# Kernel tuning notes

Hardware: AMD Instinct MI355X
Metric: run time of the kernel (lower is better)

The kernel has to match this reference:

```python
import jax, jax.numpy as jnp
import numpy as np

C = 256
NUM_HEADS = 4
REDUCTION = 4
RED = C // REDUCTION           # 64
HEAD_DIM = RED // NUM_HEADS    # 16
SCALE = HEAD_DIM ** -0.5
LN_EPS = 1e-5


def setup_inputs() -> dict:
    key = jax.random.key(0)
    ks = jax.random.split(key, 9)
    B, H, W = 2, 64, 64
    x = jax.random.normal(ks[0], (B, C, H, W), dtype=jnp.float32)
    # LayerNorm params
    norm_w = jnp.ones((C,), jnp.float32)
    norm_b = jnp.zeros((C,), jnp.float32)
    # Linear weights (torch layout: [out, in]), y = x @ W.T
    qkv_w = jax.random.normal(ks[1], (3 * RED, C), jnp.float32) * (C ** -0.5)
    out_w = jax.random.normal(ks[2], (C, RED), jnp.float32) * (RED ** -0.5)
    # 1x1 conv weights, stored as [out_c, in_c]
    conv1_w = jax.random.normal(ks[3], (C // 2, C), jnp.float32) * (C ** -0.5)
    conv1_b = jax.random.normal(ks[4], (C // 2,), jnp.float32) * 0.01
    conv2_w = jax.random.normal(ks[5], (1, C // 2), jnp.float32) * ((C // 2) ** -0.5)
    conv2_b = jax.random.normal(ks[6], (1,), jnp.float32) * 0.01
    gamma = jnp.ones((1,), jnp.float32) * 0.5  # nonzero so output depends on attention
    return {"x": x, "norm_w": norm_w, "norm_b": norm_b, "qkv_w": qkv_w,
            "out_w": out_w, "conv1_w": conv1_w, "conv1_b": conv1_b,
            "conv2_w": conv2_w, "conv2_b": conv2_b, "gamma": gamma}


def reference(x, norm_w, norm_b, qkv_w, out_w, conv1_w, conv1_b, conv2_w, conv2_b, gamma):
    B, C_, H, W = x.shape
    N = H * W
    # [B, N, C]
    xf = x.reshape(B, C_, N).transpose(0, 2, 1)
    # LayerNorm over channel dim
    mu = jnp.mean(xf, axis=-1, keepdims=True)
    var = jnp.mean(jnp.square(xf - mu), axis=-1, keepdims=True)
    xn = (xf - mu) * jax.lax.rsqrt(var + LN_EPS) * norm_w + norm_b
    # QKV projection -> [B, N, 3*RED]
    qkv = jnp.einsum('bnc,oc->bno', xn, qkv_w)
    q, k, v = jnp.split(qkv, 3, axis=-1)
    def heads(t):  # [B, N, RED] -> [B, h, N, d]
        return t.reshape(B, N, NUM_HEADS, HEAD_DIM).transpose(0, 2, 1, 3)
    q, k, v = heads(q), heads(k), heads(v)
    attn = jax.nn.softmax(jnp.einsum('bhnd,bhmd->bhnm', q, k) * SCALE, axis=-1)
    # dynamic weight branch: two 1x1 convs on raw x
    d1 = jax.nn.relu(jnp.einsum('oc,bchw->bohw', conv1_w, x) + conv1_b[None, :, None, None])
    dyn = (jnp.einsum('oc,bchw->bohw', conv2_w, d1) + conv2_b[None, :, None, None])  # [B,1,H,W]
    dyn = dyn.reshape(B, 1, N)  # broadcast over heads
    # per-query row scaling of attention
    attn = attn * dyn[:, :, :, None]
    out = jnp.einsum('bhnm,bhmd->bhnd', attn, v)            # [B,h,N,d]
    out = out.transpose(0, 2, 1, 3).reshape(B, N, RED)      # [B,N,RED]
    out = jnp.einsum('bnr,cr->bnc', out, out_w)             # [B,N,C]
    out = out.transpose(0, 2, 1).reshape(B, C_, H, W)
    return jax.nn.sigmoid(gamma[0] * out + x)
```

## Files before the change

### kernel.cpp

```cpp
#include <hip/hip_runtime.h>
#include <cstdint>
#include <cstddef>

#define LOG2E 1.44269504088896340736f

typedef float  f32x16 __attribute__((ext_vector_type(16)));
typedef __bf16 bf16x8 __attribute__((ext_vector_type(8)));

union BF8 { bf16x8 v; uint u[4]; ushort us[8]; };

__device__ __forceinline__ uint pack_bf(float a, float b) {
    uint ua = __float_as_uint(a) + 0x8000u;
    uint ub = __float_as_uint(b) + 0x8000u;
    return __builtin_amdgcn_perm(ub, ua, 0x07060302u);
}
__device__ __forceinline__ uint cvt_pk_bf(float a, float b) {
    uint r;
    asm("v_cvt_pk_bf16_f32 %0, %1, %2" : "=v"(r) : "v"(a), "v"(b));
    return r;
}
__device__ __forceinline__ float bf_lo(uint u) { return __uint_as_float(u << 16); }
__device__ __forceinline__ float bf_hi(uint u) { return __uint_as_float(u & 0xFFFF0000u); }

__global__ __launch_bounds__(256) void convert_w_kernel(
    const float* __restrict__ qkv_w, const float* __restrict__ c1w,
    const float* __restrict__ out_w,
    ushort* __restrict__ qkvw_b, ushort* __restrict__ c1w_b, ushort* __restrict__ ow_b)
{
    const int g = (blockIdx.x * 256 + threadIdx.x) * 4;
    const float* src; ushort* dst; int off; float sc = 1.f;
    if (g < 49152)      { src = qkv_w; dst = qkvw_b; off = g;
                          if (g < 16384) sc = 0.25f * LOG2E; }
    else if (g < 81920) { src = c1w;   dst = c1w_b;  off = g - 49152; }
    else                { src = out_w; dst = ow_b;   off = g - 81920; }
    float4 v = *(const float4*)(src + off);
    uint2 pk;
    pk.x = pack_bf(v.x * sc, v.y * sc);
    pk.y = pack_bf(v.z * sc, v.w * sc);
    *(uint2*)(dst + off) = pk;
}

__global__ __launch_bounds__(1024) void lnqkv_kernel(
    const float* __restrict__ x, const float* __restrict__ nw, const float* __restrict__ nb,
    const ushort* __restrict__ qkvw_b, const ushort* __restrict__ c1w_b,
    const float* __restrict__ c1b, const float* __restrict__ c2w,
    const float* __restrict__ c2b,
    ushort* __restrict__ Qb, ushort* __restrict__ Kb, ushort* __restrict__ Vsw,
    float* __restrict__ dynb)
{
    __shared__ union {
        struct {
            uint  XN[32 * 32 * 4];
            uint  XR[32 * 32 * 4];
            float red1[1024];
            float red2[1024];
        } p;
        float trans[10][33 * 32];
    } S;
    __shared__ float muS[32], rsS[32];
    __shared__ float dpart[4][32];

    const int t    = threadIdx.x;
    const int pg   = blockIdx.x;
    const int b    = pg >> 7;
    const int n0   = (pg & 127) * 32;

    {
        const int j  = t & 31;
        const int cg = t >> 5;
        const size_t xb = (size_t)b * 256 * 4096 + n0 + j;
        float v[8];
        #pragma unroll
        for (int i = 0; i < 8; ++i) v[i] = x[xb + (size_t)(cg * 8 + i) * 4096];
        float s1 = 0.f, s2 = 0.f;
        #pragma unroll
        for (int i = 0; i < 8; ++i) { s1 += v[i]; s2 += v[i] * v[i]; }
        uint4 pk;
        pk.x = pack_bf(v[0], v[1]); pk.y = pack_bf(v[2], v[3]);
        pk.z = pack_bf(v[4], v[5]); pk.w = pack_bf(v[6], v[7]);
        *(uint4*)&S.p.XR[(cg * 32 + j) * 4] = pk;
        S.p.red1[t] = s1; S.p.red2[t] = s2;
        __syncthreads();
        if (t < 32) {
            float a = 0.f, q = 0.f;
            #pragma unroll 8
            for (int g2 = 0; g2 < 32; ++g2) { a += S.p.red1[g2 * 32 + t]; q += S.p.red2[g2 * 32 + t]; }
            float mu  = a * (1.f / 256.f);
            float var = q * (1.f / 256.f) - mu * mu;
            muS[t] = mu; rsS[t] = rsqrtf(fmaxf(var, 0.f) + 1e-5f);
        }
        __syncthreads();
        const float mu = muS[j], rs = rsS[j];
        const float4 w0 = *(const float4*)(nw + cg * 8);
        const float4 w1 = *(const float4*)(nw + cg * 8 + 4);
        const float4 b0 = *(const float4*)(nb + cg * 8);
        const float4 b1 = *(const float4*)(nb + cg * 8 + 4);
        float e0 = (v[0] - mu) * rs * w0.x + b0.x;
        float e1 = (v[1] - mu) * rs * w0.y + b0.y;
        float e2 = (v[2] - mu) * rs * w0.z + b0.z;
        float e3 = (v[3] - mu) * rs * w0.w + b0.w;
        float e4 = (v[4] - mu) * rs * w1.x + b1.x;
        float e5 = (v[5] - mu) * rs * w1.y + b1.y;
        float e6 = (v[6] - mu) * rs * w1.z + b1.z;
        float e7 = (v[7] - mu) * rs * w1.w + b1.w;
        uint4 o;
        o.x = pack_bf(e0, e1); o.y = pack_bf(e2, e3);
        o.z = pack_bf(e4, e5); o.w = pack_bf(e6, e7);
        *(uint4*)&S.p.XN[(cg * 32 + j) * 4] = o;
    }
    __syncthreads();

    const int w    = t >> 6;
    const int lane = t & 63;
    const int m    = lane & 31;
    const int h    = lane >> 5;
    const ushort* xnB = (const ushort*)S.p.XN;
    const ushort* xrB = (const ushort*)S.p.XR;

    f32x16 acc;
    #pragma unroll
    for (int i = 0; i < 16; ++i) acc[i] = 0.f;

    if (w < 6) {
        const int qkv = w >> 1;
        const int ti  = w & 1;
        const ushort* ap = qkvw_b + (size_t)(qkv * 64 + ti * 32 + m) * 256 + h * 8;
        #pragma unroll 4
        for (int ks = 0; ks < 16; ++ks) {
            bf16x8 bf = *(const bf16x8*)(xnB + ((ks * 2 + h) * 32 + m) * 8);
            bf16x8 af = *(const bf16x8*)(ap + ks * 16);
            acc = __builtin_amdgcn_mfma_f32_32x32x16_bf16(af, bf, acc, 0, 0, 0);
        }
    } else if (w < 10) {
        const int ti = w - 6;
        const ushort* ap = c1w_b + (size_t)(ti * 32 + m) * 256 + h * 8;
        #pragma unroll 4
        for (int ks = 0; ks < 16; ++ks) {
            bf16x8 bf = *(const bf16x8*)(xrB + ((ks * 2 + h) * 32 + m) * 8);
            bf16x8 af = *(const bf16x8*)(ap + ks * 16);
            acc = __builtin_amdgcn_mfma_f32_32x32x16_bf16(af, bf, acc, 0, 0, 0);
        }
    }
    __syncthreads();

    if (w < 10) {
        float* tr = S.trans[w];
        #pragma unroll
        for (int r = 0; r < 16; ++r)
            tr[((r & 3) + 8 * (r >> 2) + 4 * h) * 33 + m] = acc[r];

        if (w < 4) {
            const int qkv = w >> 1, ti = w & 1;
            ushort* dst = (qkv == 0) ? Qb : Kb;
            #pragma unroll
            for (int it = 0; it < 2; ++it) {
                int unit = it * 2 + h;
                int hl = unit >> 1, half = unit & 1;
                float v0 = tr[(hl * 16 + half * 8 + 0) * 33 + m];
                float v1 = tr[(hl * 16 + half * 8 + 1) * 33 + m];
                float v2 = tr[(hl * 16 + half * 8 + 2) * 33 + m];
                float v3 = tr[(hl * 16 + half * 8 + 3) * 33 + m];
                float v4 = tr[(hl * 16 + half * 8 + 4) * 33 + m];
                float v5 = tr[(hl * 16 + half * 8 + 5) * 33 + m];
                float v6 = tr[(hl * 16 + half * 8 + 6) * 33 + m];
                float v7 = tr[(hl * 16 + half * 8 + 7) * 33 + m];
                uint4 pk;
                pk.x = pack_bf(v0, v1); pk.y = pack_bf(v2, v3);
                pk.z = pack_bf(v4, v5); pk.w = pack_bf(v6, v7);
                int head = ti * 2 + hl;
                *(uint4*)(dst + ((size_t)(b * 4 + head) * 4096 + n0 + m) * 16 + half * 8) = pk;
            }
        } else if (w < 6) {
            const int ti = w & 1;
            int d = lane & 15, u = lane >> 4;
            #pragma unroll
            for (int it = 0; it < 4; ++it) {
                int unit = it * 4 + u;
                int hl = unit >> 3, sg = unit & 7;
                float v0 = tr[(hl * 16 + d) * 33 + sg * 4 + 0];
                float v1 = tr[(hl * 16 + d) * 33 + sg * 4 + 1];
                float v2 = tr[(hl * 16 + d) * 33 + sg * 4 + 2];
                float v3 = tr[(hl * 16 + d) * 33 + sg * 4 + 3];
                uint2 pk; pk.x = pack_bf(v0, v1); pk.y = pack_bf(v2, v3);
                int head = ti * 2 + hl;
                *(uint2*)(Vsw + (((size_t)(b * 4 + head) * 1024 + (pg & 127) * 8 + sg) * 16 + d) * 4) = pk;
            }
        } else {
            const int ti = w - 6;
            float partial = 0.f;
            #pragma unroll
            for (int i = 0; i < 16; ++i) {
                int og = ti * 32 + h * 16 + i;
                partial += fmaxf(tr[(h * 16 + i) * 33 + m] + c1b[og], 0.f) * c2w[og];
            }
            float tot = partial + __shfl_xor(partial, 32);
            if (lane < 32) dpart[ti][m] = tot;
        }
    }
    __syncthreads();
    if (t < 32)
        dynb[(size_t)b * 4096 + n0 + t] =
            c2b[0] + dpart[0][t] + dpart[1][t] + dpart[2][t] + dpart[3][t];
}

__global__ __launch_bounds__(1024, 4) void attn_final_kernel(
    const ushort* __restrict__ Qb, const ushort* __restrict__ Kb,
    const ushort* __restrict__ Vsw, const float* __restrict__ dynb,
    const ushort* __restrict__ ow_b, const float* __restrict__ x,
    const float* __restrict__ gamma, float* __restrict__ out)
{
    __shared__ float2 OM[4][4][8][32];
    __shared__ float  LM[4][4][32];

    const int t    = threadIdx.x;
    const int w    = t >> 6;
    const int lane = t & 63;
    const int c    = lane & 31;
    const int h    = lane >> 5;
    const int hd   = w & 3;
    const int kb   = w >> 2;
    const int pg   = blockIdx.x;
    const int b    = pg >> 7;
    const int n0   = (pg & 127) * 32;
    const int bh   = b * 4 + hd;

    const bf16x8 qf = *(const bf16x8*)(Qb + ((size_t)bh * 4096 + n0 + c) * 16 + h * 8);

    f32x16 oacc, zf;
    #pragma unroll
    for (int i = 0; i < 16; ++i) { oacc[i] = 0.f; zf[i] = 0.f; }

    const ushort* kp = Kb + ((size_t)bh * 4096 + kb * 1024 + c) * 16 + h * 8;
    const ushort* vb = Vsw + (size_t)bh * 65536 + ((size_t)kb * 256 + h) * 64 + c * 4;

    BF8 cones;
    {
        const uint f = (c == 16) ? 0x3F803F80u : 0u;
        cones.u[0] = f; cones.u[1] = f; cones.u[2] = f; cones.u[3] = f;
    }

    bf16x8 k0 = *(const bf16x8*)kp; kp += 512;
    bf16x8 k1 = *(const bf16x8*)kp; kp += 512;
    bf16x8 k2 = *(const bf16x8*)kp; kp += 512;
    bf16x8 k3 = *(const bf16x8*)kp; kp += 512;
    uint2 vA0 = *(const uint2*)(vb),       vB0 = *(const uint2*)(vb + 128);
    uint2 vC0 = *(const uint2*)(vb + 256), vD0 = *(const uint2*)(vb + 384);
    vb += 512;
    uint2 vA1 = *(const uint2*)(vb),       vB1 = *(const uint2*)(vb + 128);
    uint2 vC1 = *(const uint2*)(vb + 256), vD1 = *(const uint2*)(vb + 384);
    vb += 512;

#define STEP(K, VA, VB, VC, VD)                                                      \
    {                                                                                \
        __builtin_amdgcn_s_setprio(1);                                               \
        f32x16 s = __builtin_amdgcn_mfma_f32_32x32x16_bf16(K, qf, zf, 0, 0, 0);      \
        __builtin_amdgcn_s_setprio(0);                                               \
        K = *(const bf16x8*)kp; kp += 512;                                           \
        BF8 p1, p2;                                                                  \
        p1.u[0] = cvt_pk_bf(__builtin_amdgcn_exp2f(s[0]),  __builtin_amdgcn_exp2f(s[1]));  \
        p1.u[1] = cvt_pk_bf(__builtin_amdgcn_exp2f(s[2]),  __builtin_amdgcn_exp2f(s[3]));  \
        p1.u[2] = cvt_pk_bf(__builtin_amdgcn_exp2f(s[4]),  __builtin_amdgcn_exp2f(s[5]));  \
        p1.u[3] = cvt_pk_bf(__builtin_amdgcn_exp2f(s[6]),  __builtin_amdgcn_exp2f(s[7]));  \
        p2.u[0] = cvt_pk_bf(__builtin_amdgcn_exp2f(s[8]),  __builtin_amdgcn_exp2f(s[9]));  \
        p2.u[1] = cvt_pk_bf(__builtin_amdgcn_exp2f(s[10]), __builtin_amdgcn_exp2f(s[11])); \
        p2.u[2] = cvt_pk_bf(__builtin_amdgcn_exp2f(s[12]), __builtin_amdgcn_exp2f(s[13])); \
        p2.u[3] = cvt_pk_bf(__builtin_amdgcn_exp2f(s[14]), __builtin_amdgcn_exp2f(s[15])); \
        BF8 a1, a2;                                                                  \
        if (c < 16) {                                                                \
            a1.u[0] = VA.x; a1.u[1] = VA.y; a1.u[2] = VB.x; a1.u[3] = VB.y;          \
            a2.u[0] = VC.x; a2.u[1] = VC.y; a2.u[2] = VD.x; a2.u[3] = VD.y;          \
        } else { a1 = cones; a2 = cones; }                                           \
        VA = *(const uint2*)(vb);       VB = *(const uint2*)(vb + 128);              \
        VC = *(const uint2*)(vb + 256); VD = *(const uint2*)(vb + 384);              \
        vb += 512;                                                                   \
        __builtin_amdgcn_s_setprio(1);                                               \
        oacc = __builtin_amdgcn_mfma_f32_32x32x16_bf16(a1.v, p1.v, oacc, 0, 0, 0);   \
        oacc = __builtin_amdgcn_mfma_f32_32x32x16_bf16(a2.v, p2.v, oacc, 0, 0, 0);   \
        __builtin_amdgcn_s_setprio(0);                                               \
    }

    for (int it = 0; it < 8; ++it) {
        STEP(k0, vA0, vB0, vC0, vD0);
        STEP(k1, vA1, vB1, vC1, vD1);
        STEP(k2, vA0, vB0, vC0, vD0);
        STEP(k3, vA1, vB1, vC1, vD1);
    }
#undef STEP

    OM[kb][hd][2 * h + 0][c] = make_float2(oacc[0], oacc[1]);
    OM[kb][hd][2 * h + 1][c] = make_float2(oacc[2], oacc[3]);
    OM[kb][hd][4 + 2 * h][c] = make_float2(oacc[4], oacc[5]);
    OM[kb][hd][5 + 2 * h][c] = make_float2(oacc[6], oacc[7]);
    if (h == 0) LM[kb][hd][c] = oacc[8];
    __syncthreads();

    if (w < 8) {
        const int m = c;
        const float dyn_px = dynb[(size_t)b * 4096 + n0 + m];

        f32x16 acc;
        #pragma unroll
        for (int i = 0; i < 16; ++i) acc[i] = 0.f;

        #pragma unroll
        for (int ks = 0; ks < 4; ++ks) {
            float l = LM[0][ks][m] + LM[1][ks][m] + LM[2][ks][m] + LM[3][ks][m];
            float fac = dyn_px / l;
            BF8 bfr;
            #pragma unroll
            for (int i = 0; i < 4; ++i) {
                int sl = 4 * h + i;
                float2 s0 = OM[0][ks][sl][m];
                float2 s1 = OM[1][ks][sl][m];
                float2 s2 = OM[2][ks][sl][m];
                float2 s3 = OM[3][ks][sl][m];
                float e0 = (s0.x + s1.x + s2.x + s3.x) * fac;
                float e1 = (s0.y + s1.y + s2.y + s3.y) * fac;
                bfr.u[i] = pack_bf(e0, e1);
            }
            bf16x8 af = *(const bf16x8*)(ow_b + (size_t)(w * 32 + m) * 64 + ks * 16 + h * 8);
            acc = __builtin_amdgcn_mfma_f32_32x32x16_bf16(af, bfr.v, acc, 0, 0, 0);
        }

        const float g = gamma[0];
        #pragma unroll
        for (int r = 0; r < 16; ++r) {
            int o = (r & 3) + 8 * (r >> 2) + 4 * h;
            size_t idx = ((size_t)b * 256 + w * 32 + o) * 4096 + n0 + m;
            float z = g * acc[r] + x[idx];
            out[idx] = 1.f / (1.f + __builtin_amdgcn_exp2f(-z * LOG2E));
        }
    }
}

extern "C" void kernel_launch(void* const* d_in, const int* in_sizes, int n_in,
                              void* d_out, int out_size, void* d_ws, size_t ws_size,
                              hipStream_t stream)
{
    const float* x      = (const float*)d_in[0];
    const float* norm_w = (const float*)d_in[1];
    const float* norm_b = (const float*)d_in[2];
    const float* qkv_w  = (const float*)d_in[3];
    const float* out_w  = (const float*)d_in[4];
    const float* c1w    = (const float*)d_in[5];
    const float* c1b    = (const float*)d_in[6];
    const float* c2w    = (const float*)d_in[7];
    const float* c2b    = (const float*)d_in[8];
    const float* gamma  = (const float*)d_in[9];

    char* ws = (char*)d_ws;
    ushort* Qb     = (ushort*)ws;
    ushort* Kb     = Qb + 524288;
    ushort* Vsw    = Kb + 524288;
    ushort* qkvw_b = Vsw + 524288;
    ushort* c1w_b  = qkvw_b + 49152;
    ushort* ow_b   = c1w_b + 32768;
    float*  dynb   = (float*)(ws + 3342336);

    hipLaunchKernelGGL(convert_w_kernel, dim3(96), dim3(256), 0, stream,
                       qkv_w, c1w, out_w, qkvw_b, c1w_b, ow_b);
    hipLaunchKernelGGL(lnqkv_kernel, dim3(256), dim3(1024), 0, stream,
                       x, norm_w, norm_b, qkvw_b, c1w_b, c1b, c2w, c2b,
                       Qb, Kb, Vsw, dynb);
    hipLaunchKernelGGL(attn_final_kernel, dim3(256), dim3(1024), 0, stream,
                       Qb, Kb, Vsw, dynb, ow_b, x, gamma, (float*)d_out);
}
```

Baseline: 113.5 us.

## Fuse LN/QKV and attention kernels into one cooperative launch with grid sync

Merges the LayerNorm+QKV projection kernel and the attention+output kernel into a single cooperative kernel separated by a grid-wide barrier, with shared memory for both phases overlaid in a union. This removes one kernel launch and the inter-kernel gap. In exchange, all 256 blocks of 1024 threads must be co-resident, and a grid sync plus threadfence is added. The attention phase's occupancy hint of 4 blocks per CU now also constrains the first phase's register budget.

```diff
diff --git a/kernel.cpp b/kernel.cpp
--- a/kernel.cpp
+++ b/kernel.cpp
@@ -1,6 +1,9 @@
 #include <hip/hip_runtime.h>
+#include <hip/hip_cooperative_groups.h>
 #include <cstdint>
 #include <cstddef>
+
+namespace cg = cooperative_groups;
 
 #define LOG2E 1.44269504088896340736f
 
@@ -19,8 +22,6 @@
     asm("v_cvt_pk_bf16_f32 %0, %1, %2" : "=v"(r) : "v"(a), "v"(b));
     return r;
 }
-__device__ __forceinline__ float bf_lo(uint u) { return __uint_as_float(u << 16); }
-__device__ __forceinline__ float bf_hi(uint u) { return __uint_as_float(u & 0xFFFF0000u); }
 
 __global__ __launch_bounds__(256) void convert_w_kernel(
     const float* __restrict__ qkv_w, const float* __restrict__ c1w,
@@ -40,295 +41,294 @@
     *(uint2*)(dst + off) = pk;
 }
 
-__global__ __launch_bounds__(1024) void lnqkv_kernel(
+__global__ __launch_bounds__(1024, 4) void fused_kernel(
     const float* __restrict__ x, const float* __restrict__ nw, const float* __restrict__ nb,
     const ushort* __restrict__ qkvw_b, const ushort* __restrict__ c1w_b,
     const float* __restrict__ c1b, const float* __restrict__ c2w,
     const float* __restrict__ c2b,
     ushort* __restrict__ Qb, ushort* __restrict__ Kb, ushort* __restrict__ Vsw,
-    float* __restrict__ dynb)
+    float* __restrict__ dynb,
+    const ushort* __restrict__ ow_b, const float* __restrict__ gamma,
+    float* __restrict__ out)
 {
     __shared__ union {
         struct {
-            uint  XN[32 * 32 * 4];
-            uint  XR[32 * 32 * 4];
-            float red1[1024];
-            float red2[1024];
-        } p;
-        float trans[10][33 * 32];
-    } S;
-    __shared__ float muS[32], rsS[32];
-    __shared__ float dpart[4][32];
+            union {
+                struct {
+                    uint  XN[32 * 32 * 4];
+                    uint  XR[32 * 32 * 4];
+                    float red1[1024];
+                    float red2[1024];
+                } p;
+                float trans[10][33 * 32];
+            } S;
+            float muS[32], rsS[32];
+            float dpart[4][32];
+        } ln;
+        struct {
+            float2 OM[4][4][8][32];
+            float  LM[4][4][32];
+        } at;
+    } U;
 
     const int t    = threadIdx.x;
     const int pg   = blockIdx.x;
     const int b    = pg >> 7;
     const int n0   = (pg & 127) * 32;
-
-    {
-        const int j  = t & 31;
-        const int cg = t >> 5;
-        const size_t xb = (size_t)b * 256 * 4096 + n0 + j;
-        float v[8];
-        #pragma unroll
-        for (int i = 0; i < 8; ++i) v[i] = x[xb + (size_t)(cg * 8 + i) * 4096];
-        float s1 = 0.f, s2 = 0.f;
-        #pragma unroll
-        for (int i = 0; i < 8; ++i) { s1 += v[i]; s2 += v[i] * v[i]; }
-        uint4 pk;
-        pk.x = pack_bf(v[0], v[1]); pk.y = pack_bf(v[2], v[3]);
-        pk.z = pack_bf(v[4], v[5]); pk.w = pack_bf(v[6], v[7]);
-        *(uint4*)&S.p.XR[(cg * 32 + j) * 4] = pk;
-        S.p.red1[t] = s1; S.p.red2[t] = s2;
-        __syncthreads();
-        if (t < 32) {
-            float a = 0.f, q = 0.f;
-            #pragma unroll 8
-            for (int g2 = 0; g2 < 32; ++g2) { a += S.p.red1[g2 * 32 + t]; q += S.p.red2[g2 * 32 + t]; }
-            float mu  = a * (1.f / 256.f);
-            float var = q * (1.f / 256.f) - mu * mu;
-            muS[t] = mu; rsS[t] = rsqrtf(fmaxf(var, 0.f) + 1e-5f);
-        }
-        __syncthreads();
-        const float mu = muS[j], rs = rsS[j];
-        const float4 w0 = *(const float4*)(nw + cg * 8);
-        const float4 w1 = *(const float4*)(nw + cg * 8 + 4);
-        const float4 b0 = *(const float4*)(nb + cg * 8);
-        const float4 b1 = *(const float4*)(nb + cg * 8 + 4);
-        float e0 = (v[0] - mu) * rs * w0.x + b0.x;
-        float e1 = (v[1] - mu) * rs * w0.y + b0.y;
-        float e2 = (v[2] - mu) * rs * w0.z + b0.z;
-        float e3 = (v[3] - mu) * rs * w0.w + b0.w;
-        float e4 = (v[4] - mu) * rs * w1.x + b1.x;
-        float e5 = (v[5] - mu) * rs * w1.y + b1.y;
-        float e6 = (v[6] - mu) * rs * w1.z + b1.z;
-        float e7 = (v[7] - mu) * rs * w1.w + b1.w;
-        uint4 o;
-        o.x = pack_bf(e0, e1); o.y = pack_bf(e2, e3);
-        o.z = pack_bf(e4, e5); o.w = pack_bf(e6, e7);
-        *(uint4*)&S.p.XN[(cg * 32 + j) * 4] = o;
-    }
-    __syncthreads();
-
     const int w    = t >> 6;
     const int lane = t & 63;
     const int m    = lane & 31;
     const int h    = lane >> 5;
-    const ushort* xnB = (const ushort*)S.p.XN;
-    const ushort* xrB = (const ushort*)S.p.XR;
-
-    f32x16 acc;
-    #pragma unroll
-    for (int i = 0; i < 16; ++i) acc[i] = 0.f;
-
-    if (w < 6) {
-        const int qkv = w >> 1;
-        const int ti  = w & 1;
-        const ushort* ap = qkvw_b + (size_t)(qkv * 64 + ti * 32 + m) * 256 + h * 8;
-        #pragma unroll 4
-        for (int ks = 0; ks < 16; ++ks) {
-            bf16x8 bf = *(const bf16x8*)(xnB + ((ks * 2 + h) * 32 + m) * 8);
-            bf16x8 af = *(const bf16x8*)(ap + ks * 16);
-            acc = __builtin_amdgcn_mfma_f32_32x32x16_bf16(af, bf, acc, 0, 0, 0);
-        }
-    } else if (w < 10) {
-        const int ti = w - 6;
-        const ushort* ap = c1w_b + (size_t)(ti * 32 + m) * 256 + h * 8;
-        #pragma unroll 4
-        for (int ks = 0; ks < 16; ++ks) {
-            bf16x8 bf = *(const bf16x8*)(xrB + ((ks * 2 + h) * 32 + m) * 8);
-            bf16x8 af = *(const bf16x8*)(ap + ks * 16);
-            acc = __builtin_amdgcn_mfma_f32_32x32x16_bf16(af, bf, acc, 0, 0, 0);
-        }
-    }
-    __syncthreads();
-
-    if (w < 10) {
-        float* tr = S.trans[w];
-        #pragma unroll
-        for (int r = 0; r < 16; ++r)
-            tr[((r & 3) + 8 * (r >> 2) + 4 * h) * 33 + m] = acc[r];
-
-        if (w < 4) {
-            const int qkv = w >> 1, ti = w & 1;
-            ushort* dst = (qkv == 0) ? Qb : Kb;
-            #pragma unroll
-            for (int it = 0; it < 2; ++it) {
-                int unit = it * 2 + h;
-                int hl = unit >> 1, half = unit & 1;
-                float v0 = tr[(hl * 16 + half * 8 + 0) * 33 + m];
-                float v1 = tr[(hl * 16 + half * 8 + 1) * 33 + m];
-                float v2 = tr[(hl * 16 + half * 8 + 2) * 33 + m];
-                float v3 = tr[(hl * 16 + half * 8 + 3) * 33 + m];
-                float v4 = tr[(hl * 16 + half * 8 + 4) * 33 + m];
-                float v5 = tr[(hl * 16 + half * 8 + 5) * 33 + m];
-                float v6 = tr[(hl * 16 + half * 8 + 6) * 33 + m];
-                float v7 = tr[(hl * 16 + half * 8 + 7) * 33 + m];
-                uint4 pk;
-                pk.x = pack_bf(v0, v1); pk.y = pack_bf(v2, v3);
-                pk.z = pack_bf(v4, v5); pk.w = pack_bf(v6, v7);
-                int head = ti * 2 + hl;
-                *(uint4*)(dst + ((size_t)(b * 4 + head) * 4096 + n0 + m) * 16 + half * 8) = pk;
-            }
-        } else if (w < 6) {
-            const int ti = w & 1;
-            int d = lane & 15, u = lane >> 4;
-            #pragma unroll
-            for (int it = 0; it < 4; ++it) {
-                int unit = it * 4 + u;
-                int hl = unit >> 3, sg = unit & 7;
-                float v0 = tr[(hl * 16 + d) * 33 + sg * 4 + 0];
-                float v1 = tr[(hl * 16 + d) * 33 + sg * 4 + 1];
-                float v2 = tr[(hl * 16 + d) * 33 + sg * 4 + 2];
-                float v3 = tr[(hl * 16 + d) * 33 + sg * 4 + 3];
-                uint2 pk; pk.x = pack_bf(v0, v1); pk.y = pack_bf(v2, v3);
-                int head = ti * 2 + hl;
-                *(uint2*)(Vsw + (((size_t)(b * 4 + head) * 1024 + (pg & 127) * 8 + sg) * 16 + d) * 4) = pk;
-            }
-        } else {
-            const int ti = w - 6;
-            float partial = 0.f;
-            #pragma unroll
-            for (int i = 0; i < 16; ++i) {
-                int og = ti * 32 + h * 16 + i;
-                partial += fmaxf(tr[(h * 16 + i) * 33 + m] + c1b[og], 0.f) * c2w[og];
-            }
-            float tot = partial + __shfl_xor(partial, 32);
-            if (lane < 32) dpart[ti][m] = tot;
-        }
-    }
-    __syncthreads();
-    if (t < 32)
-        dynb[(size_t)b * 4096 + n0 + t] =
-            c2b[0] + dpart[0][t] + dpart[1][t] + dpart[2][t] + dpart[3][t];
-}
-
-__global__ __launch_bounds__(1024, 4) void attn_final_kernel(
-    const ushort* __restrict__ Qb, const ushort* __restrict__ Kb,
-    const ushort* __restrict__ Vsw, const float* __restrict__ dynb,
-    const ushort* __restrict__ ow_b, const float* __restrict__ x,
-    const float* __restrict__ gamma, float* __restrict__ out)
-{
-    __shared__ float2 OM[4][4][8][32];
-    __shared__ float  LM[4][4][32];
-
-    const int t    = threadIdx.x;
-    const int w    = t >> 6;
-    const int lane = t & 63;
-    const int c    = lane & 31;
-    const int h    = lane >> 5;
-    const int hd   = w & 3;
-    const int kb   = w >> 2;
-    const int pg   = blockIdx.x;
-    const int b    = pg >> 7;
-    const int n0   = (pg & 127) * 32;
-    const int bh   = b * 4 + hd;
-
-    const bf16x8 qf = *(const bf16x8*)(Qb + ((size_t)bh * 4096 + n0 + c) * 16 + h * 8);
-
-    f32x16 oacc, zf;
-    #pragma unroll
-    for (int i = 0; i < 16; ++i) { oacc[i] = 0.f; zf[i] = 0.f; }
-
-    const ushort* kp = Kb + ((size_t)bh * 4096 + kb * 1024 + c) * 16 + h * 8;
-    const ushort* vb = Vsw + (size_t)bh * 65536 + ((size_t)kb * 256 + h) * 64 + c * 4;
-
-    BF8 cones;
+
     {
-        const uint f = (c == 16) ? 0x3F803F80u : 0u;
-        cones.u[0] = f; cones.u[1] = f; cones.u[2] = f; cones.u[3] = f;
-    }
-
-    bf16x8 k0 = *(const bf16x8*)kp; kp += 512;
-    bf16x8 k1 = *(const bf16x8*)kp; kp += 512;
-    bf16x8 k2 = *(const bf16x8*)kp; kp += 512;
-    bf16x8 k3 = *(const bf16x8*)kp; kp += 512;
-    uint2 vA0 = *(const uint2*)(vb),       vB0 = *(const uint2*)(vb + 128);
-    uint2 vC0 = *(const uint2*)(vb + 256), vD0 = *(const uint2*)(vb + 384);
-    vb += 512;
-    uint2 vA1 = *(const uint2*)(vb),       vB1 = *(const uint2*)(vb + 128);
-    uint2 vC1 = *(const uint2*)(vb + 256), vD1 = *(const uint2*)(vb + 384);
-    vb += 512;
-
-#define STEP(K, VA, VB, VC, VD)                                                      \
-    {                                                                                \
-        __builtin_amdgcn_s_setprio(1);                                               \
-        f32x16 s = __builtin_amdgcn_mfma_f32_32x32x16_bf16(K, qf, zf, 0, 0, 0);      \
-        __builtin_amdgcn_s_setprio(0);                                               \
-        K = *(const bf16x8*)kp; kp += 512;                                           \
-        BF8 p1, p2;                                                                  \
-        p1.u[0] = cvt_pk_bf(__builtin_amdgcn_exp2f(s[0]),  __builtin_amdgcn_exp2f(s[1]));  \
-        p1.u[1] = cvt_pk_bf(__builtin_amdgcn_exp2f(s[2]),  __builtin_amdgcn_exp2f(s[3]));  \
-        p1.u[2] = cvt_pk_bf(__builtin_amdgcn_exp2f(s[4]),  __builtin_amdgcn_exp2f(s[5]));  \
-        p1.u[3] = cvt_pk_bf(__builtin_amdgcn_exp2f(s[6]),  __builtin_amdgcn_exp2f(s[7]));  \
-        p2.u[0] = cvt_pk_bf(__builtin_amdgcn_exp2f(s[8]),  __builtin_amdgcn_exp2f(s[9]));  \
-        p2.u[1] = cvt_pk_bf(__builtin_amdgcn_exp2f(s[10]), __builtin_amdgcn_exp2f(s[11])); \
-        p2.u[2] = cvt_pk_bf(__builtin_amdgcn_exp2f(s[12]), __builtin_amdgcn_exp2f(s[13])); \
-        p2.u[3] = cvt_pk_bf(__builtin_amdgcn_exp2f(s[14]), __builtin_amdgcn_exp2f(s[15])); \
-        BF8 a1, a2;                                                                  \
-        if (c < 16) {                                                                \
-            a1.u[0] = VA.x; a1.u[1] = VA.y; a1.u[2] = VB.x; a1.u[3] = VB.y;          \
-            a2.u[0] = VC.x; a2.u[1] = VC.y; a2.u[2] = VD.x; a2.u[3] = VD.y;          \
-        } else { a1 = cones; a2 = cones; }                                           \
-        VA = *(const uint2*)(vb);       VB = *(const uint2*)(vb + 128);              \
-        VC = *(const uint2*)(vb + 256); VD = *(const uint2*)(vb + 384);              \
-        vb += 512;                                                                   \
-        __builtin_amdgcn_s_setprio(1);                                               \
-        oacc = __builtin_amdgcn_mfma_f32_32x32x16_bf16(a1.v, p1.v, oacc, 0, 0, 0);   \
-        oacc = __builtin_amdgcn_mfma_f32_32x32x16_bf16(a2.v, p2.v, oacc, 0, 0, 0);   \
-        __builtin_amdgcn_s_setprio(0);                                               \
-    }
-
-    for (int it = 0; it < 8; ++it) {
-        STEP(k0, vA0, vB0, vC0, vD0);
-        STEP(k1, vA1, vB1, vC1, vD1);
-        STEP(k2, vA0, vB0, vC0, vD0);
-        STEP(k3, vA1, vB1, vC1, vD1);
-    }
-#undef STEP
-
-    OM[kb][hd][2 * h + 0][c] = make_float2(oacc[0], oacc[1]);
-    OM[kb][hd][2 * h + 1][c] = make_float2(oacc[2], oacc[3]);
-    OM[kb][hd][4 + 2 * h][c] = make_float2(oacc[4], oacc[5]);
-    OM[kb][hd][5 + 2 * h][c] = make_float2(oacc[6], oacc[7]);
-    if (h == 0) LM[kb][hd][c] = oacc[8];
-    __syncthreads();
-
-    if (w < 8) {
-        const int m = c;
-        const float dyn_px = dynb[(size_t)b * 4096 + n0 + m];
+        {
+            const int j  = t & 31;
+            const int cg2 = t >> 5;
+            const size_t xb = (size_t)b * 256 * 4096 + n0 + j;
+            float v[8];
+            #pragma unroll
+            for (int i = 0; i < 8; ++i) v[i] = x[xb + (size_t)(cg2 * 8 + i) * 4096];
+            float s1 = 0.f, s2 = 0.f;
+            #pragma unroll
+            for (int i = 0; i < 8; ++i) { s1 += v[i]; s2 += v[i] * v[i]; }
+            uint4 pk;
+            pk.x = pack_bf(v[0], v[1]); pk.y = pack_bf(v[2], v[3]);
+            pk.z = pack_bf(v[4], v[5]); pk.w = pack_bf(v[6], v[7]);
+            *(uint4*)&U.ln.S.p.XR[(cg2 * 32 + j) * 4] = pk;
+            U.ln.S.p.red1[t] = s1; U.ln.S.p.red2[t] = s2;
+            __syncthreads();
+            if (t < 32) {
+                float a = 0.f, q = 0.f;
+                #pragma unroll 8
+                for (int g2 = 0; g2 < 32; ++g2) { a += U.ln.S.p.red1[g2 * 32 + t]; q += U.ln.S.p.red2[g2 * 32 + t]; }
+                float mu  = a * (1.f / 256.f);
+                float var = q * (1.f / 256.f) - mu * mu;
+                U.ln.muS[t] = mu; U.ln.rsS[t] = rsqrtf(fmaxf(var, 0.f) + 1e-5f);
+            }
+            __syncthreads();
+            const float mu = U.ln.muS[j], rs = U.ln.rsS[j];
+            const float4 w0 = *(const float4*)(nw + cg2 * 8);
+            const float4 w1 = *(const float4*)(nw + cg2 * 8 + 4);
+            const float4 b0 = *(const float4*)(nb + cg2 * 8);
+            const float4 b1 = *(const float4*)(nb + cg2 * 8 + 4);
+            float e0 = (v[0] - mu) * rs * w0.x + b0.x;
+            float e1 = (v[1] - mu) * rs * w0.y + b0.y;
+            float e2 = (v[2] - mu) * rs * w0.z + b0.z;
+            float e3 = (v[3] - mu) * rs * w0.w + b0.w;
+            float e4 = (v[4] - mu) * rs * w1.x + b1.x;
+            float e5 = (v[5] - mu) * rs * w1.y + b1.y;
+            float e6 = (v[6] - mu) * rs * w1.z + b1.z;
+            float e7 = (v[7] - mu) * rs * w1.w + b1.w;
+            uint4 o;
+            o.x = pack_bf(e0, e1); o.y = pack_bf(e2, e3);
+            o.z = pack_bf(e4, e5); o.w = pack_bf(e6, e7);
+            *(uint4*)&U.ln.S.p.XN[(cg2 * 32 + j) * 4] = o;
+        }
+        __syncthreads();
+
+        const ushort* xnB = (const ushort*)U.ln.S.p.XN;
+        const ushort* xrB = (const ushort*)U.ln.S.p.XR;
 
         f32x16 acc;
         #pragma unroll
         for (int i = 0; i < 16; ++i) acc[i] = 0.f;
 
+        if (w < 6) {
+            const int qkv = w >> 1;
+            const int ti  = w & 1;
+            const ushort* ap = qkvw_b + (size_t)(qkv * 64 + ti * 32 + m) * 256 + h * 8;
+            #pragma unroll 4
+            for (int ks = 0; ks < 16; ++ks) {
+                bf16x8 bf = *(const bf16x8*)(xnB + ((ks * 2 + h) * 32 + m) * 8);
+                bf16x8 af = *(const bf16x8*)(ap + ks * 16);
+                acc = __builtin_amdgcn_mfma_f32_32x32x16_bf16(af, bf, acc, 0, 0, 0);
+            }
+        } else if (w < 10) {
+            const int ti = w - 6;
+            const ushort* ap = c1w_b + (size_t)(ti * 32 + m) * 256 + h * 8;
+            #pragma unroll 4
+            for (int ks = 0; ks < 16; ++ks) {
+                bf16x8 bf = *(const bf16x8*)(xrB + ((ks * 2 + h) * 32 + m) * 8);
+                bf16x8 af = *(const bf16x8*)(ap + ks * 16);
+                acc = __builtin_amdgcn_mfma_f32_32x32x16_bf16(af, bf, acc, 0, 0, 0);
+            }
+        }
+        __syncthreads();
+
+        if (w < 10) {
+            float* tr = U.ln.S.trans[w];
+            #pragma unroll
+            for (int r = 0; r < 16; ++r)
+                tr[((r & 3) + 8 * (r >> 2) + 4 * h) * 33 + m] = acc[r];
+
+            if (w < 4) {
+                const int qkv = w >> 1, ti = w & 1;
+                ushort* dst = (qkv == 0) ? Qb : Kb;
+                #pragma unroll
+                for (int it = 0; it < 2; ++it) {
+                    int unit = it * 2 + h;
+                    int hl = unit >> 1, half = unit & 1;
+                    float v0 = tr[(hl * 16 + half * 8 + 0) * 33 + m];
+                    float v1 = tr[(hl * 16 + half * 8 + 1) * 33 + m];
+                    float v2 = tr[(hl * 16 + half * 8 + 2) * 33 + m];
+                    float v3 = tr[(hl * 16 + half * 8 + 3) * 33 + m];
+                    float v4 = tr[(hl * 16 + half * 8 + 4) * 33 + m];
+                    float v5 = tr[(hl * 16 + half * 8 + 5) * 33 + m];
+                    float v6 = tr[(hl * 16 + half * 8 + 6) * 33 + m];
+                    float v7 = tr[(hl * 16 + half * 8 + 7) * 33 + m];
+                    uint4 pk;
+                    pk.x = pack_bf(v0, v1); pk.y = pack_bf(v2, v3);
+                    pk.z = pack_bf(v4, v5); pk.w = pack_bf(v6, v7);
+                    int head = ti * 2 + hl;
+                    *(uint4*)(dst + ((size_t)(b * 4 + head) * 4096 + n0 + m) * 16 + half * 8) = pk;
+                }
+            } else if (w < 6) {
+                const int ti = w & 1;
+                int d = lane & 15, u = lane >> 4;
+                #pragma unroll
+                for (int it = 0; it < 4; ++it) {
+                    int unit = it * 4 + u;
+                    int hl = unit >> 3, sg = unit & 7;
+                    float v0 = tr[(hl * 16 + d) * 33 + sg * 4 + 0];
+                    float v1 = tr[(hl * 16 + d) * 33 + sg * 4 + 1];
+                    float v2 = tr[(hl * 16 + d) * 33 + sg * 4 + 2];
+                    float v3 = tr[(hl * 16 + d) * 33 + sg * 4 + 3];
+                    uint2 pk; pk.x = pack_bf(v0, v1); pk.y = pack_bf(v2, v3);
+                    int head = ti * 2 + hl;
+                    *(uint2*)(Vsw + (((size_t)(b * 4 + head) * 1024 + (pg & 127) * 8 + sg) * 16 + d) * 4) = pk;
+                }
+            } else {
+                const int ti = w - 6;
+                float partial = 0.f;
+                #pragma unroll
+                for (int i = 0; i < 16; ++i) {
+                    int og = ti * 32 + h * 16 + i;
+                    partial += fmaxf(tr[(h * 16 + i) * 33 + m] + c1b[og], 0.f) * c2w[og];
+                }
+                float tot = partial + __shfl_xor(partial, 32);
+                if (lane < 32) U.ln.dpart[ti][m] = tot;
+            }
+        }
+        __syncthreads();
+        if (t < 32)
+            dynb[(size_t)b * 4096 + n0 + t] =
+                c2b[0] + U.ln.dpart[0][t] + U.ln.dpart[1][t] + U.ln.dpart[2][t] + U.ln.dpart[3][t];
+    }
+
+    __threadfence();
+    cg::this_grid().sync();
+
+    {
+        const int c    = lane & 31;
+        const int hd   = w & 3;
+        const int kb   = w >> 2;
+        const int bh   = b * 4 + hd;
+
+        const bf16x8 qf = *(const bf16x8*)(Qb + ((size_t)bh * 4096 + n0 + c) * 16 + h * 8);
+
+        f32x16 oacc, zf;
         #pragma unroll
-        for (int ks = 0; ks < 4; ++ks) {
-            float l = LM[0][ks][m] + LM[1][ks][m] + LM[2][ks][m] + LM[3][ks][m];
-            float fac = dyn_px / l;
-            BF8 bfr;
-            #pragma unroll
-            for (int i = 0; i < 4; ++i) {
-                int sl = 4 * h + i;
-                float2 s0 = OM[0][ks][sl][m];
-                float2 s1 = OM[1][ks][sl][m];
-                float2 s2 = OM[2][ks][sl][m];
-                float2 s3 = OM[3][ks][sl][m];
-                float e0 = (s0.x + s1.x + s2.x + s3.x) * fac;
-                float e1 = (s0.y + s1.y + s2.y + s3.y) * fac;
-                bfr.u[i] = pack_bf(e0, e1);
-            }
-            bf16x8 af = *(const bf16x8*)(ow_b + (size_t)(w * 32 + m) * 64 + ks * 16 + h * 8);
-            acc = __builtin_amdgcn_mfma_f32_32x32x16_bf16(af, bfr.v, acc, 0, 0, 0);
-        }
-
-        const float g = gamma[0];
-        #pragma unroll
-        for (int r = 0; r < 16; ++r) {
-            int o = (r & 3) + 8 * (r >> 2) + 4 * h;
-            size_t idx = ((size_t)b * 256 + w * 32 + o) * 4096 + n0 + m;
-            float z = g * acc[r] + x[idx];
-            out[idx] = 1.f / (1.f + __builtin_amdgcn_exp2f(-z * LOG2E));
+        for (int i = 0; i < 16; ++i) { oacc[i] = 0.f; zf[i] = 0.f; }
+
+        const ushort* kp = Kb + ((size_t)bh * 4096 + kb * 1024 + c) * 16 + h * 8;
+        const ushort* vb = Vsw + (size_t)bh * 65536 + ((size_t)kb * 256 + h) * 64 + c * 4;
+
+        BF8 cones;
+        {
+            const uint f = (c == 16) ? 0x3F803F80u : 0u;
+            cones.u[0] = f; cones.u[1] = f; cones.u[2] = f; cones.u[3] = f;
+        }
+
+        bf16x8 k0 = *(const bf16x8*)kp; kp += 512;
+        bf16x8 k1 = *(const bf16x8*)kp; kp += 512;
+        bf16x8 k2 = *(const bf16x8*)kp; kp += 512;
+        bf16x8 k3 = *(const bf16x8*)kp; kp += 512;
+        uint2 vA0 = *(const uint2*)(vb),       vB0 = *(const uint2*)(vb + 128);
+        uint2 vC0 = *(const uint2*)(vb + 256), vD0 = *(const uint2*)(vb + 384);
+        vb += 512;
+        uint2 vA1 = *(const uint2*)(vb),       vB1 = *(const uint2*)(vb + 128);
+        uint2 vC1 = *(const uint2*)(vb + 256), vD1 = *(const uint2*)(vb + 384);
+        vb += 512;
+
+#define STEP(K, VA, VB, VC, VD)                                                      \
+        {                                                                            \
+            __builtin_amdgcn_s_setprio(1);                                           \
+            f32x16 s = __builtin_amdgcn_mfma_f32_32x32x16_bf16(K, qf, zf, 0, 0, 0);  \
+            __builtin_amdgcn_s_setprio(0);                                           \
+            K = *(const bf16x8*)kp; kp += 512;                                       \
+            BF8 p1, p2;                                                              \
+            p1.u[0] = cvt_pk_bf(__builtin_amdgcn_exp2f(s[0]),  __builtin_amdgcn_exp2f(s[1]));  \
+            p1.u[1] = cvt_pk_bf(__builtin_amdgcn_exp2f(s[2]),  __builtin_amdgcn_exp2f(s[3]));  \
+            p1.u[2] = cvt_pk_bf(__builtin_amdgcn_exp2f(s[4]),  __builtin_amdgcn_exp2f(s[5]));  \
+            p1.u[3] = cvt_pk_bf(__builtin_amdgcn_exp2f(s[6]),  __builtin_amdgcn_exp2f(s[7]));  \
+            p2.u[0] = cvt_pk_bf(__builtin_amdgcn_exp2f(s[8]),  __builtin_amdgcn_exp2f(s[9]));  \
+            p2.u[1] = cvt_pk_bf(__builtin_amdgcn_exp2f(s[10]), __builtin_amdgcn_exp2f(s[11])); \
+            p2.u[2] = cvt_pk_bf(__builtin_amdgcn_exp2f(s[12]), __builtin_amdgcn_exp2f(s[13])); \
+            p2.u[3] = cvt_pk_bf(__builtin_amdgcn_exp2f(s[14]), __builtin_amdgcn_exp2f(s[15])); \
+            BF8 a1, a2;                                                              \
+            if (c < 16) {                                                            \
+                a1.u[0] = VA.x; a1.u[1] = VA.y; a1.u[2] = VB.x; a1.u[3] = VB.y;      \
+                a2.u[0] = VC.x; a2.u[1] = VC.y; a2.u[2] = VD.x; a2.u[3] = VD.y;      \
+            } else { a1 = cones; a2 = cones; }                                       \
+            VA = *(const uint2*)(vb);       VB = *(const uint2*)(vb + 128);          \
+            VC = *(const uint2*)(vb + 256); VD = *(const uint2*)(vb + 384);          \
+            vb += 512;                                                               \
+            __builtin_amdgcn_s_setprio(1);                                           \
+            oacc = __builtin_amdgcn_mfma_f32_32x32x16_bf16(a1.v, p1.v, oacc, 0, 0, 0); \
+            oacc = __builtin_amdgcn_mfma_f32_32x32x16_bf16(a2.v, p2.v, oacc, 0, 0, 0); \
+            __builtin_amdgcn_s_setprio(0);                                           \
+        }
+
+        for (int it = 0; it < 8; ++it) {
+            STEP(k0, vA0, vB0, vC0, vD0);
+            STEP(k1, vA1, vB1, vC1, vD1);
+            STEP(k2, vA0, vB0, vC0, vD0);
+            STEP(k3, vA1, vB1, vC1, vD1);
+        }
+#undef STEP
+
+        U.at.OM[kb][hd][2 * h + 0][c] = make_float2(oacc[0], oacc[1]);
+        U.at.OM[kb][hd][2 * h + 1][c] = make_float2(oacc[2], oacc[3]);
+        U.at.OM[kb][hd][4 + 2 * h][c] = make_float2(oacc[4], oacc[5]);
+        U.at.OM[kb][hd][5 + 2 * h][c] = make_float2(oacc[6], oacc[7]);
+        if (h == 0) U.at.LM[kb][hd][c] = oacc[8];
+        __syncthreads();
+
+        if (w < 8) {
+            const float dyn_px = dynb[(size_t)b * 4096 + n0 + m];
+
+            f32x16 acc;
+            #pragma unroll
+            for (int i = 0; i < 16; ++i) acc[i] = 0.f;
+
+            #pragma unroll
+            for (int ks = 0; ks < 4; ++ks) {
+                float l = U.at.LM[0][ks][m] + U.at.LM[1][ks][m] + U.at.LM[2][ks][m] + U.at.LM[3][ks][m];
+                float fac = dyn_px / l;
+                BF8 bfr;
+                #pragma unroll
+                for (int i = 0; i < 4; ++i) {
+                    int sl = 4 * h + i;
+                    float2 s0 = U.at.OM[0][ks][sl][m];
+                    float2 s1 = U.at.OM[1][ks][sl][m];
+                    float2 s2 = U.at.OM[2][ks][sl][m];
+                    float2 s3 = U.at.OM[3][ks][sl][m];
+                    float e0 = (s0.x + s1.x + s2.x + s3.x) * fac;
+                    float e1 = (s0.y + s1.y + s2.y + s3.y) * fac;
+                    bfr.u[i] = pack_bf(e0, e1);
+                }
+                bf16x8 af = *(const bf16x8*)(ow_b + (size_t)(w * 32 + m) * 64 + ks * 16 + h * 8);
+                acc = __builtin_amdgcn_mfma_f32_32x32x16_bf16(af, bfr.v, acc, 0, 0, 0);
+            }
+
+            const float g = gamma[0];
+            #pragma unroll
+            for (int r = 0; r < 16; ++r) {
+                int o = (r & 3) + 8 * (r >> 2) + 4 * h;
+                size_t idx = ((size_t)b * 256 + w * 32 + o) * 4096 + n0 + m;
+                float z = g * acc[r] + x[idx];
+                out[idx] = 1.f / (1.f + __builtin_amdgcn_exp2f(-z * LOG2E));
+            }
         }
     }
 }
@@ -356,12 +356,18 @@
     ushort* c1w_b  = qkvw_b + 49152;
     ushort* ow_b   = c1w_b + 32768;
     float*  dynb   = (float*)(ws + 3342336);
+    float*  outp   = (float*)d_out;
 
     hipLaunchKernelGGL(convert_w_kernel, dim3(96), dim3(256), 0, stream,
                        qkv_w, c1w, out_w, qkvw_b, c1w_b, ow_b);
-    hipLaunchKernelGGL(lnqkv_kernel, dim3(256), dim3(1024), 0, stream,
-                       x, norm_w, norm_b, qkvw_b, c1w_b, c1b, c2w, c2b,
-                       Qb, Kb, Vsw, dynb);
-    hipLaunchKernelGGL(attn_final_kernel, dim3(256), dim3(1024), 0, stream,
-                       Qb, Kb, Vsw, dynb, ow_b, x, gamma, (float*)d_out);
-}
+
+    void* args[] = {
+        (void*)&x, (void*)&norm_w, (void*)&norm_b,
+        (void*)&qkvw_b, (void*)&c1w_b,
+        (void*)&c1b, (void*)&c2w, (void*)&c2b,
+        (void*)&Qb, (void*)&Kb, (void*)&Vsw, (void*)&dynb,
+        (void*)&ow_b, (void*)&gamma, (void*)&outp
+    };
+    hipLaunchCooperativeKernel((const void*)fused_kernel, dim3(256), dim3(1024),
+                               args, 0, stream);
+}
```

Measured after the change: 210.8 us. +85.8%, slower.
